# Optimization experiments

Hardware: AMD Instinct MI355X
Metric: run time of the kernel (lower is better)

## Reference

```python
import jax, jax.numpy as jnp
import numpy as np

N = 50000   # nodes
D = 128     # feature / out_channels
E = 800000  # edges per edge type
L = 2       # num_layers
T = 2       # num edge types


def setup_inputs() -> dict:
    key = jax.random.key(0)
    ks = jax.random.split(key, 6)
    x = jax.random.normal(ks[0], (N, D), dtype=jnp.float32)
    h = jax.random.normal(ks[1], (N, D), dtype=jnp.float32)  # unused by forward, kept for fidelity
    edge_index_a = jax.random.randint(ks[2], (2, E), 0, N)
    edge_index_b = jax.random.randint(ks[3], (2, E), 0, N)
    Wl = (jax.random.normal(ks[4], (L, T, D, D), dtype=jnp.float32) * 0.05)
    bl = jnp.zeros((L, T, D), dtype=jnp.float32)
    Wr = (jax.random.normal(ks[5], (L, T, D, D), dtype=jnp.float32) * 0.05)
    return {"x": x, "h": h, "edge_index_a": edge_index_a, "edge_index_b": edge_index_b,
            "Wl": Wl, "bl": bl, "Wr": Wr}


def _sage(x, edge_index, Wl, bl, Wr):
    # PyG SAGEConv: lin_l(mean_{j->i} x_j) + lin_r(x_i); lin_l has bias, lin_r does not.
    src, dst = edge_index[0], edge_index[1]
    msg_sum = jax.ops.segment_sum(x[src], dst, num_segments=N)            # [N, D]
    deg = jax.ops.segment_sum(jnp.ones((edge_index.shape[1],), x.dtype), dst, num_segments=N)
    mean = msg_sum / jnp.maximum(deg, 1.0)[:, None]
    return mean @ Wl + bl + x @ Wr


def reference(x, h, edge_index_a, edge_index_b, Wl, bl, Wr):
    out = x
    for l in range(L):
        # HeteroConv default aggregation: sum over edge types with same dst node type
        out = (_sage(out, edge_index_a, Wl[l, 0], bl[l, 0], Wr[l, 0])
               + _sage(out, edge_index_b, Wl[l, 1], bl[l, 1], Wr[l, 1]))
    return jax.nn.sigmoid(out)
```

## Files before the change

### kernel.cpp

```cpp
#include <hip/hip_runtime.h>
#include <math.h>

#define N_NODES 50000
#define D 128
#define NE 800000
#define BN 64
#define NBUCK 782
#define CAP 1280
#define EPB 4096
#define PBLK 196
#define F2B_BLKS 6250
#define WPREP_BLKS 384
#define MPITCH 68

typedef unsigned int uint;
typedef unsigned short ushort;

using bf16x8 = __attribute__((ext_vector_type(8))) short;
using f32x4  = __attribute__((ext_vector_type(4))) float;

__device__ __forceinline__ float bflo(uint w) {
    union { uint u; float f; } c; c.u = w << 16; return c.f;
}
__device__ __forceinline__ float bfhi(uint w) {
    union { uint u; float f; } c; c.u = w & 0xffff0000u; return c.f;
}
__device__ __forceinline__ uint fp2bf_rn(float f) {
    union { float f; uint u; } c; c.f = f;
    return (c.u + 0x7fffu + ((c.u >> 16) & 1u)) >> 16;
}

__global__ __launch_bounds__(256) void build_kernel(
    const float4* __restrict__ x4, uint2* __restrict__ featb2,
    const float* __restrict__ Wl, const float* __restrict__ Wr,
    ushort* __restrict__ Wpack,
    const int* __restrict__ srcA, const int* __restrict__ dstA,
    const int* __restrict__ srcB, const int* __restrict__ dstB,
    int* __restrict__ bcurA, int* __restrict__ bcurB,
    uint* __restrict__ ebufA, uint* __restrict__ ebufB) {
    const int blk = blockIdx.x;
    const int t   = threadIdx.x;
    if (blk < 2 * PBLK) {
        __shared__ int h[NBUCK];
        __shared__ int base[NBUCK];
        const int typ = blk >= PBLK;
        const int* src = typ ? srcB : srcA;
        const int* dst = typ ? dstB : dstA;
        int* bc        = typ ? bcurB : bcurA;
        uint* ebuf     = typ ? ebufB : ebufA;
        const int e0 = (blk - (typ ? PBLK : 0)) * EPB;
        for (int j = t; j < NBUCK; j += 256) h[j] = 0;
        __syncthreads();
#pragma unroll
        for (int i = 0; i < EPB / 256; ++i) {
            const int e = e0 + t + i * 256;
            if (e < NE) atomicAdd(&h[dst[e] >> 6], 1);
        }
        __syncthreads();
        for (int j = t; j < NBUCK; j += 256) {
            const int c = h[j];
            base[j] = c ? atomicAdd(&bc[j], c) : 0;
            h[j] = 0;
        }
        __syncthreads();
#pragma unroll
        for (int i = 0; i < EPB / 256; ++i) {
            const int e = e0 + t + i * 256;
            if (e < NE) {
                const int d  = dst[e];
                const int bk = d >> 6;
                const int pos = atomicAdd(&h[bk], 1);
                const int off = base[bk] + pos;
                if (off < CAP)
                    ebuf[(size_t)bk * CAP + off] = (uint)src[e] | ((uint)(d & 63) << 17);
            }
        }
    } else if (blk < 2 * PBLK + F2B_BLKS) {
        const int i = (blk - 2 * PBLK) * 256 + t;
        float4 v = x4[i];
        uint2 o;
        o.x = fp2bf_rn(v.x) | (fp2bf_rn(v.y) << 16);
        o.y = fp2bf_rn(v.z) | (fp2bf_rn(v.w) << 16);
        featb2[i] = o;
    } else {
        const int i   = (blk - 2 * PBLK - F2B_BLKS) * 256 + t;
        const int l   = i / 49152;
        const int rem = i % 49152;
        const int ks  = rem / 4096;
        const int n   = (rem % 4096) / 32;
        const int kk  = rem % 32;
        const int r   = ks * 32 + kk;
        float v;
        if (r < 128)       v = Wl[(((size_t)l * 2 + 0) * 128 + r) * 128 + n];
        else if (r < 256)  v = Wl[(((size_t)l * 2 + 1) * 128 + (r - 128)) * 128 + n];
        else               v = Wr[(((size_t)l * 2 + 0) * 128 + (r - 256)) * 128 + n]
                             + Wr[(((size_t)l * 2 + 1) * 128 + (r - 256)) * 128 + n];
        Wpack[i] = (ushort)fp2bf_rn(v);
    }
}

__global__ __launch_bounds__(1024, 8) void fused_kernel(
    const uint4* __restrict__ feat,
    const uint* __restrict__ ebufA, const uint* __restrict__ ebufB,
    const int* __restrict__ bcntA, const int* __restrict__ bcntB,
    const ushort* __restrict__ Wpack,
    const float* __restrict__ bias0, const float* __restrict__ bias1,
    float* __restrict__ outf, ushort* __restrict__ outb, int act) {

    __shared__ uint   mlds[2 * BN * MPITCH];
    __shared__ ushort lidx[2][CAP];
    __shared__ int    cnt[128], ex[128], cur[128];

    const int b = blockIdx.x;
    const int t = threadIdx.x;

    if (t < 128) cnt[t] = 0;
    __syncthreads();
    int countA = bcntA[b]; if (countA > CAP) countA = CAP;
    int countB = bcntB[b]; if (countB > CAP) countB = CAP;
    const uint* ebA = ebufA + (size_t)b * CAP;
    const uint* ebB = ebufB + (size_t)b * CAP;
    for (int e = t; e < countA; e += 1024) atomicAdd(&cnt[ebA[e] >> 17], 1);
    for (int e = t; e < countB; e += 1024) atomicAdd(&cnt[64 + (ebB[e] >> 17)], 1);
    __syncthreads();
    if (t < 128) ex[t] = cnt[t];
    __syncthreads();
    for (int off = 1; off < 64; off <<= 1) {
        int v = 0;
        if (t < 128 && (t & 63) >= off) v = ex[t - off];
        __syncthreads();
        if (t < 128 && (t & 63) >= off) ex[t] += v;
        __syncthreads();
    }
    if (t < 128) { ex[t] -= cnt[t]; cur[t] = ex[t]; }
    __syncthreads();
    for (int e = t; e < countA; e += 1024) {
        const uint rec = ebA[e];
        const int p = atomicAdd(&cur[rec >> 17], 1);
        lidx[0][p] = (ushort)(rec & 0x1FFFFu);
    }
    for (int e = t; e < countB; e += 1024) {
        const uint rec = ebB[e];
        const int p = atomicAdd(&cur[64 + (rec >> 17)], 1);
        lidx[1][p] = (ushort)(rec & 0x1FFFFu);
    }
    __syncthreads();

    const int cl = t >> 4, ln = t & 15;
#pragma unroll
    for (int typ = 0; typ < 2; ++typ) {
        const int beg = ex[typ * 64 + cl];
        const int fin = beg + cnt[typ * 64 + cl];
        const ushort* lx = lidx[typ];
        float a[8] = {0.f,0.f,0.f,0.f,0.f,0.f,0.f,0.f};
#define ACC(v) { a[0]+=bflo(v.x); a[1]+=bfhi(v.x); a[2]+=bflo(v.y); a[3]+=bfhi(v.y); \
                 a[4]+=bflo(v.z); a[5]+=bfhi(v.z); a[6]+=bflo(v.w); a[7]+=bfhi(v.w); }
        int e = beg;
        for (; e + 4 <= fin; e += 4) {
            uint4 v0 = feat[(size_t)lx[e]     * 16 + ln];
            uint4 v1 = feat[(size_t)lx[e + 1] * 16 + ln];
            uint4 v2 = feat[(size_t)lx[e + 2] * 16 + ln];
            uint4 v3 = feat[(size_t)lx[e + 3] * 16 + ln];
            ACC(v0); ACC(v1); ACC(v2); ACC(v3);
        }
        for (; e < fin; ++e) {
            uint4 v0 = feat[(size_t)lx[e] * 16 + ln];
            ACC(v0);
        }
#undef ACC
        const float invd = 1.0f / fmaxf((float)(fin - beg), 1.0f);
        uint4 o;
        o.x = fp2bf_rn(a[0] * invd) | (fp2bf_rn(a[1] * invd) << 16);
        o.y = fp2bf_rn(a[2] * invd) | (fp2bf_rn(a[3] * invd) << 16);
        o.z = fp2bf_rn(a[4] * invd) | (fp2bf_rn(a[5] * invd) << 16);
        o.w = fp2bf_rn(a[6] * invd) | (fp2bf_rn(a[7] * invd) << 16);
        *reinterpret_cast<uint4*>(&mlds[(typ * BN + cl) * MPITCH + ln * 4]) = o;
    }
    __syncthreads();

    const int wid = t >> 6, wl = t & 63;
    const int mrow = wl & 15, g = wl >> 4;
    const int mt   = wid >> 2;
    const int ntp  = (wid & 3) * 2;
    const int arow = mt * 16 + mrow;

    f32x4 acc0 = (f32x4){0.f, 0.f, 0.f, 0.f};
    f32x4 acc1 = (f32x4){0.f, 0.f, 0.f, 0.f};
#pragma unroll
    for (int ks = 0; ks < 12; ++ks) {
        union { uint4 u; bf16x8 v; } av;
        if (ks < 8) {
            av.u = *reinterpret_cast<const uint4*>(
                &mlds[((ks >> 2) * BN + arow) * MPITCH + (ks & 3) * 16 + g * 4]);
        } else {
            int srow = b * BN + arow;
            if (srow >= N_NODES) srow = N_NODES - 1;
            av.u = feat[(size_t)srow * 16 + (ks & 3) * 4 + g];
        }
        const ushort* Wk = Wpack + (size_t)ks * 128 * 32;
        union { uint4 u; bf16x8 v; } bv0, bv1;
        bv0.u = *reinterpret_cast<const uint4*>(Wk + ((ntp * 16 + mrow) * 32 + g * 8));
        bv1.u = *reinterpret_cast<const uint4*>(Wk + (((ntp + 1) * 16 + mrow) * 32 + g * 8));
        acc0 = __builtin_amdgcn_mfma_f32_16x16x32_bf16(av.v, bv0.v, acc0, 0, 0, 0);
        acc1 = __builtin_amdgcn_mfma_f32_16x16x32_bf16(av.v, bv1.v, acc1, 0, 0, 0);
    }

#pragma unroll
    for (int q = 0; q < 2; ++q) {
        const f32x4 av = q ? acc1 : acc0;
        const int col = (ntp + q) * 16 + mrow;
        const float bias = bias0[col] + bias1[col];
#pragma unroll
        for (int r = 0; r < 4; ++r) {
            const int row = b * BN + mt * 16 + g * 4 + r;
            if (row < N_NODES) {
                const float v = av[r] + bias;
                if (act) outf[(size_t)row * D + col] = 1.0f / (1.0f + expf(-v));
                else     outb[(size_t)row * D + col] = (ushort)fp2bf_rn(v);
            }
        }
    }
}

extern "C" void kernel_launch(void* const* d_in, const int* in_sizes, int n_in,
                              void* d_out, int out_size, void* d_ws, size_t ws_size,
                              hipStream_t stream) {
    const float* x    = (const float*)d_in[0];
    const int*   ei_a = (const int*)d_in[2];
    const int*   ei_b = (const int*)d_in[3];
    const float* Wl   = (const float*)d_in[4];
    const float* bl   = (const float*)d_in[5];
    const float* Wr   = (const float*)d_in[6];
    float* out = (float*)d_out;

    ushort* featb = (ushort*)d_ws;
    ushort* feat2 = featb + (size_t)N_NODES * D;
    uint* ebufA = (uint*)(feat2 + (size_t)N_NODES * D);
    uint* ebufB = ebufA + (size_t)NBUCK * CAP;
    int* bcurA  = (int*)(ebufB + (size_t)NBUCK * CAP);
    int* bcurB  = bcurA + NBUCK;
    ushort* Wpack = (ushort*)(((size_t)(bcurB + NBUCK) + 63) & ~(size_t)63);

    const int* srcA = ei_a;
    const int* dstA = ei_a + NE;
    const int* srcB = ei_b;
    const int* dstB = ei_b + NE;

    hipMemsetAsync(bcurA, 0, 2ull * NBUCK * sizeof(int), stream);
    build_kernel<<<2 * PBLK + F2B_BLKS + WPREP_BLKS, 256, 0, stream>>>(
        (const float4*)x, (uint2*)featb, Wl, Wr, Wpack,
        srcA, dstA, srcB, dstB, bcurA, bcurB, ebufA, ebufB);

    fused_kernel<<<NBUCK, 1024, 0, stream>>>(
        (const uint4*)featb, ebufA, ebufB, bcurA, bcurB,
        Wpack, bl + 0 * D, bl + 1 * D, nullptr, feat2, 0);
    fused_kernel<<<NBUCK, 1024, 0, stream>>>(
        (const uint4*)feat2, ebufA, ebufB, bcurA, bcurB,
        Wpack + (size_t)12 * 128 * 32, bl + 2 * D, bl + 3 * D, out, nullptr, 1);
}
```

Before: 203.2 us.

## Split each destination bucket across two blocks to increase parallelism

Each fused block now handles 32 destination nodes instead of 64, and the grid doubles. Blocks filter the shared bucket edge lists by half, gather both edge types concurrently with one thread group per node-type pair, and each wave computes one MFMA output tile. This aims to shorten per-thread serial gather work and improve latency hiding, at the cost of scanning edge buffers and loading weights twice. A smaller per-half edge capacity adds a truncation risk.

Measured after the change: 205.4 us. No clear change (+1.1%).

```diff
diff --git a/kernel.cpp b/kernel.cpp
--- a/kernel.cpp
+++ b/kernel.cpp
@@ -7,6 +7,9 @@
 #define BN 64
 #define NBUCK 782
 #define CAP 1280
+#define HB 32
+#define NHALF 1564
+#define CAP_H 704
 #define EPB 4096
 #define PBLK 196
 #define F2B_BLKS 6250
@@ -107,50 +110,64 @@
     const float* __restrict__ bias0, const float* __restrict__ bias1,
     float* __restrict__ outf, ushort* __restrict__ outb, int act) {
 
-    __shared__ uint   mlds[2 * BN * MPITCH];
-    __shared__ ushort lidx[2][CAP];
-    __shared__ int    cnt[128], ex[128], cur[128];
-
-    const int b = blockIdx.x;
-    const int t = threadIdx.x;
-
-    if (t < 128) cnt[t] = 0;
+    __shared__ uint   mlds[2 * HB * MPITCH];
+    __shared__ ushort lidx[2][CAP_H];
+    __shared__ int    cnt[64], ex[64], cur[64];
+
+    const int bq = blockIdx.x;
+    const int b  = bq >> 1;
+    const int q  = bq & 1;
+    const int t  = threadIdx.x;
+
+    if (t < 64) cnt[t] = 0;
     __syncthreads();
     int countA = bcntA[b]; if (countA > CAP) countA = CAP;
     int countB = bcntB[b]; if (countB > CAP) countB = CAP;
     const uint* ebA = ebufA + (size_t)b * CAP;
     const uint* ebB = ebufB + (size_t)b * CAP;
-    for (int e = t; e < countA; e += 1024) atomicAdd(&cnt[ebA[e] >> 17], 1);
-    for (int e = t; e < countB; e += 1024) atomicAdd(&cnt[64 + (ebB[e] >> 17)], 1);
-    __syncthreads();
-    if (t < 128) ex[t] = cnt[t];
-    __syncthreads();
-    for (int off = 1; off < 64; off <<= 1) {
-        int v = 0;
-        if (t < 128 && (t & 63) >= off) v = ex[t - off];
-        __syncthreads();
-        if (t < 128 && (t & 63) >= off) ex[t] += v;
-        __syncthreads();
-    }
-    if (t < 128) { ex[t] -= cnt[t]; cur[t] = ex[t]; }
-    __syncthreads();
     for (int e = t; e < countA; e += 1024) {
         const uint rec = ebA[e];
-        const int p = atomicAdd(&cur[rec >> 17], 1);
-        lidx[0][p] = (ushort)(rec & 0x1FFFFu);
+        if ((int)((rec >> 17) >> 5) == q) atomicAdd(&cnt[(rec >> 17) & 31], 1);
     }
     for (int e = t; e < countB; e += 1024) {
         const uint rec = ebB[e];
-        const int p = atomicAdd(&cur[64 + (rec >> 17)], 1);
-        lidx[1][p] = (ushort)(rec & 0x1FFFFu);
+        if ((int)((rec >> 17) >> 5) == q) atomicAdd(&cnt[32 + ((rec >> 17) & 31)], 1);
+    }
+    __syncthreads();
+    if (t < 64) ex[t] = cnt[t];
+    __syncthreads();
+    for (int off = 1; off < 32; off <<= 1) {
+        int v = 0;
+        if (t < 64 && (t & 31) >= off) v = ex[t - off];
+        __syncthreads();
+        if (t < 64 && (t & 31) >= off) ex[t] += v;
+        __syncthreads();
+    }
+    if (t < 64) { ex[t] -= cnt[t]; cur[t] = ex[t]; }
+    __syncthreads();
+    for (int e = t; e < countA; e += 1024) {
+        const uint rec = ebA[e];
+        if ((int)((rec >> 17) >> 5) == q) {
+            const int p = atomicAdd(&cur[(rec >> 17) & 31], 1);
+            if (p < CAP_H) lidx[0][p] = (ushort)(rec & 0x1FFFFu);
+        }
+    }
+    for (int e = t; e < countB; e += 1024) {
+        const uint rec = ebB[e];
+        if ((int)((rec >> 17) >> 5) == q) {
+            const int p = atomicAdd(&cur[32 + ((rec >> 17) & 31)], 1);
+            if (p < CAP_H) lidx[1][p] = (ushort)(rec & 0x1FFFFu);
+        }
     }
     __syncthreads();
 
     const int cl = t >> 4, ln = t & 15;
-#pragma unroll
-    for (int typ = 0; typ < 2; ++typ) {
-        const int beg = ex[typ * 64 + cl];
-        const int fin = beg + cnt[typ * 64 + cl];
+    {
+        const int typ   = cl >> 5;
+        const int lnode = cl & 31;
+        const int beg   = ex[typ * 32 + lnode];
+        const int deg   = cnt[typ * 32 + lnode];
+        int fin = beg + deg; if (fin > CAP_H) fin = CAP_H;
         const ushort* lx = lidx[typ];
         float a[8] = {0.f,0.f,0.f,0.f,0.f,0.f,0.f,0.f};
 #define ACC(v) { a[0]+=bflo(v.x); a[1]+=bfhi(v.x); a[2]+=bflo(v.y); a[3]+=bfhi(v.y); \
@@ -168,53 +185,48 @@
             ACC(v0);
         }
 #undef ACC
-        const float invd = 1.0f / fmaxf((float)(fin - beg), 1.0f);
+        const float invd = 1.0f / fmaxf((float)deg, 1.0f);
         uint4 o;
         o.x = fp2bf_rn(a[0] * invd) | (fp2bf_rn(a[1] * invd) << 16);
         o.y = fp2bf_rn(a[2] * invd) | (fp2bf_rn(a[3] * invd) << 16);
         o.z = fp2bf_rn(a[4] * invd) | (fp2bf_rn(a[5] * invd) << 16);
         o.w = fp2bf_rn(a[6] * invd) | (fp2bf_rn(a[7] * invd) << 16);
-        *reinterpret_cast<uint4*>(&mlds[(typ * BN + cl) * MPITCH + ln * 4]) = o;
+        *reinterpret_cast<uint4*>(&mlds[(typ * HB + cl % 32) * MPITCH + ln * 4]) = o;
     }
     __syncthreads();
 
     const int wid = t >> 6, wl = t & 63;
     const int mrow = wl & 15, g = wl >> 4;
-    const int mt   = wid >> 2;
-    const int ntp  = (wid & 3) * 2;
+    const int mt = wid >> 3;
+    const int nf = wid & 7;
     const int arow = mt * 16 + mrow;
 
-    f32x4 acc0 = (f32x4){0.f, 0.f, 0.f, 0.f};
-    f32x4 acc1 = (f32x4){0.f, 0.f, 0.f, 0.f};
+    f32x4 acc = (f32x4){0.f, 0.f, 0.f, 0.f};
 #pragma unroll
     for (int ks = 0; ks < 12; ++ks) {
         union { uint4 u; bf16x8 v; } av;
         if (ks < 8) {
             av.u = *reinterpret_cast<const uint4*>(
-                &mlds[((ks >> 2) * BN + arow) * MPITCH + (ks & 3) * 16 + g * 4]);
+                &mlds[((ks >> 2) * HB + arow) * MPITCH + (ks & 3) * 16 + g * 4]);
         } else {
-            int srow = b * BN + arow;
+            int srow = bq * HB + arow;
             if (srow >= N_NODES) srow = N_NODES - 1;
             av.u = feat[(size_t)srow * 16 + (ks & 3) * 4 + g];
         }
-        const ushort* Wk = Wpack + (size_t)ks * 128 * 32;
-        union { uint4 u; bf16x8 v; } bv0, bv1;
-        bv0.u = *reinterpret_cast<const uint4*>(Wk + ((ntp * 16 + mrow) * 32 + g * 8));
-        bv1.u = *reinterpret_cast<const uint4*>(Wk + (((ntp + 1) * 16 + mrow) * 32 + g * 8));
-        acc0 = __builtin_amdgcn_mfma_f32_16x16x32_bf16(av.v, bv0.v, acc0, 0, 0, 0);
-        acc1 = __builtin_amdgcn_mfma_f32_16x16x32_bf16(av.v, bv1.v, acc1, 0, 0, 0);
-    }
-
-#pragma unroll
-    for (int q = 0; q < 2; ++q) {
-        const f32x4 av = q ? acc1 : acc0;
-        const int col = (ntp + q) * 16 + mrow;
+        union { uint4 u; bf16x8 v; } bv;
+        bv.u = *reinterpret_cast<const uint4*>(
+            Wpack + (size_t)ks * 4096 + ((nf * 16 + mrow) * 32 + g * 8));
+        acc = __builtin_amdgcn_mfma_f32_16x16x32_bf16(av.v, bv.v, acc, 0, 0, 0);
+    }
+
+    {
+        const int col = nf * 16 + mrow;
         const float bias = bias0[col] + bias1[col];
 #pragma unroll
         for (int r = 0; r < 4; ++r) {
-            const int row = b * BN + mt * 16 + g * 4 + r;
+            const int row = bq * HB + mt * 16 + g * 4 + r;
             if (row < N_NODES) {
-                const float v = av[r] + bias;
+                const float v = acc[r] + bias;
                 if (act) outf[(size_t)row * D + col] = 1.0f / (1.0f + expf(-v));
                 else     outb[(size_t)row * D + col] = (ushort)fp2bf_rn(v);
             }
@@ -251,10 +263,10 @@
         (const float4*)x, (uint2*)featb, Wl, Wr, Wpack,
         srcA, dstA, srcB, dstB, bcurA, bcurB, ebufA, ebufB);
 
-    fused_kernel<<<NBUCK, 1024, 0, stream>>>(
+    fused_kernel<<<NHALF, 1024, 0, stream>>>(
         (const uint4*)featb, ebufA, ebufB, bcurA, bcurB,
         Wpack, bl + 0 * D, bl + 1 * D, nullptr, feat2, 0);
-    fused_kernel<<<NBUCK, 1024, 0, stream>>>(
+    fused_kernel<<<NHALF, 1024, 0, stream>>>(
         (const uint4*)feat2, ebufA, ebufB, bcurA, bcurB,
         Wpack + (size_t)12 * 128 * 32, bl + 2 * D, bl + 3 * D, out, nullptr, 1);
 }
```
